# Kernel tuning notes

Measured on AMD Instinct MI355X. Metric: run time of the kernel, lower is better.

## Reference

```python
import jax, jax.numpy as jnp
import numpy as np

B, N, D, H, C = 2, 2048, 1024, 16, 3
Dh = D // H


def setup_inputs() -> dict:
    key = jax.random.key(0)
    ks = jax.random.split(key, 6)
    x = jax.random.normal(ks[0], (B, N, D), jnp.float32)
    coords = jax.random.normal(ks[1], (B, N, C), jnp.float32)
    attn_mask = jax.random.normal(ks[2], (N, N), jnp.float32) * 0.1  # additive float bias (2d kind)
    Wqkv = jax.random.normal(ks[3], (D, 3 * D), jnp.float32) / np.sqrt(D)
    bqkv = jax.random.normal(ks[4], (3 * D,), jnp.float32) * 0.01
    rel_weight = jax.random.normal(ks[5], (H, C), jnp.float32) * 0.02
    return {"x": x, "coords": coords, "attn_mask": attn_mask,
            "Wqkv": Wqkv, "bqkv": bqkv, "rel_weight": rel_weight}


def reference(x, coords, attn_mask, Wqkv, bqkv, rel_weight):
    b, n, d = x.shape
    h, dh = rel_weight.shape[0], d // rel_weight.shape[0]
    scale = 1.0 / np.sqrt(float(dh))

    qkv = x @ Wqkv + bqkv                      # [B,N,3D]
    q, k, v = jnp.split(qkv, 3, axis=-1)

    def to_heads(t):
        return t.reshape(b, n, h, dh).transpose(0, 2, 1, 3)  # [B,H,N,Dh]

    qh, kh, vh = to_heads(q), to_heads(k), to_heads(v)

    # scaled dot-product scores (flex_attention applies scale before score_mod)
    scores = jnp.einsum('bhnd,bhmd->bhnm', qh, kh) * scale   # [B,H,N,N]

    # coordinate-derived per-head relative bias: coord_proj[b,h,qi] - coord_proj[b,h,kj]
    coord_proj = jnp.einsum('bnc,hc->bhn', coords.astype(jnp.float32), rel_weight)
    scores = scores + coord_proj[:, :, :, None] - coord_proj[:, :, None, :]

    # additive float mask bias, '2d' kind: shape (N,N) broadcast over B,H
    scores = scores + attn_mask[None, None, :, :]

    attn = jax.nn.softmax(scores, axis=-1)
    out = jnp.einsum('bhnm,bhmd->bhnd', attn, vh)            # [B,H,N,Dh]
    return out.transpose(0, 2, 1, 3).reshape(b, n, d)        # [B,N,D]
```

## Files before the change

### kernel.cpp

```cpp
#include <hip/hip_runtime.h>

typedef _Float16 half8 __attribute__((ext_vector_type(8)));
typedef _Float16 half4 __attribute__((ext_vector_type(4)));
typedef float floatx4 __attribute__((ext_vector_type(4)));


__device__ __forceinline__ void async16(const void* g, void* l) {
    __builtin_amdgcn_global_load_lds(
        (const __attribute__((address_space(1))) unsigned int*)g,
        (__attribute__((address_space(3))) unsigned int*)l, 16, 0, 0);
}

__global__ void k_convert_x(const float* __restrict__ x, _Float16* __restrict__ xh) {
    int i = blockIdx.x * blockDim.x + threadIdx.x;
    const floatx4* xin = (const floatx4*)x;
    floatx4 a = xin[i * 2];
    floatx4 b = xin[i * 2 + 1];
    half8 h;
    h[0] = (_Float16)a[0]; h[1] = (_Float16)a[1]; h[2] = (_Float16)a[2]; h[3] = (_Float16)a[3];
    h[4] = (_Float16)b[0]; h[5] = (_Float16)b[1]; h[6] = (_Float16)b[2]; h[7] = (_Float16)b[3];
    *(half8*)&xh[i * 8] = h;
}

__global__ void k_transpose_w(const float* __restrict__ W, _Float16* __restrict__ Wt) {
    __shared__ float tile[32][33];
    int n0 = blockIdx.x * 32, k0 = blockIdx.y * 32;
    int tx = threadIdx.x, ty = threadIdx.y;
    #pragma unroll
    for (int r = 0; r < 4; ++r)
        tile[ty + r * 8][tx] = W[(k0 + ty + r * 8) * 3072 + n0 + tx];
    __syncthreads();
    #pragma unroll
    for (int r = 0; r < 4; ++r)
        Wt[(n0 + ty + r * 8) * 1024 + k0 + tx] = (_Float16)tile[tx][ty + r * 8];
}

__global__ void k_negcp(const float* __restrict__ coords, const float* __restrict__ rw,
                        float* __restrict__ negcp) {
    int idx = blockIdx.x * 256 + threadIdx.x;
    int bh = idx >> 11, n = idx & 2047;
    int b = bh >> 4, h = bh & 15;
    const float* c = &coords[(b * 2048 + n) * 3];
    const float* w = &rw[h * 3];
    negcp[idx] = -(c[0] * w[0] + c[1] * w[1] + c[2] * w[2]);
}

__global__ void k_prep_mask(const float* __restrict__ mask, _Float16* __restrict__ maskp) {
    int gid = blockIdx.x * 256 + threadIdx.x;
    int lane = gid & 63, t = (gid >> 6) & 3, w = (gid >> 8) & 3;
    int kt = (gid >> 10) & 31, qt = gid >> 15;
    int quad = lane >> 4, l16 = lane & 15;
    int row = qt * 64 + w * 16 + l16;
    int col = kt * 64 + t * 16 + quad * 4;
    floatx4 m = *(const floatx4*)&mask[row * 2048 + col];
    half4 v;
    #pragma unroll
    for (int i = 0; i < 4; ++i) v[i] = (_Float16)m[i];
    ((half4*)maskp)[gid] = v;
}

__global__ __launch_bounds__(256) void k_gemm(
    const _Float16* __restrict__ Ah, const _Float16* __restrict__ Bt,
    const float* __restrict__ bias,
    _Float16* __restrict__ qh, _Float16* __restrict__ kh, _Float16* __restrict__ vt) {
    __shared__ _Float16 smem[18432];
    _Float16* As = smem;
    _Float16* Bs = smem + 8192;
    int tid = threadIdx.x;
    int w = tid >> 6, lane = tid & 63;
    int quad = lane >> 4, l16 = lane & 15;
    int m0 = blockIdx.y * 128;
    int n0 = blockIdx.x * 128;
    bool QK = n0 < 2048;
    int mq = (w >> 1) * 64, nq = (w & 1) * 64;
    int c0 = n0 + nq;

    int rl = lane >> 3;
    int pb = lane & 7;
    floatx4 acc[4][4] = {};

    for (int kt = 0; kt < 16; ++kt) {
        #pragma unroll
        for (int j = 0; j < 4; ++j) {
            int row = w * 32 + j * 8 + rl;
            async16(&Ah[(size_t)(m0 + row) * 1024 + kt * 64 + ((pb ^ (row & 7)) << 3)],
                    &As[(w * 32 + j * 8) * 64]);
            async16(&Bt[(size_t)(n0 + row) * 1024 + kt * 64 + ((pb ^ (row & 7)) << 3)],
                    &Bs[(w * 32 + j * 8) * 64]);
        }
        __syncthreads();
        #pragma unroll
        for (int kc = 0; kc < 2; ++kc) {
            half8 af[4], bf[4];
            #pragma unroll
            for (int s = 0; s < 4; ++s) {
                int ra = mq + s * 16 + l16;
                af[s] = *(const half8*)&As[ra * 64 + ((((kc << 2) + quad) ^ (ra & 7)) << 3)];
                int rb = nq + s * 16 + l16;
                bf[s] = *(const half8*)&Bs[rb * 64 + ((((kc << 2) + quad) ^ (rb & 7)) << 3)];
            }
            if (QK) {
                #pragma unroll
                for (int ms = 0; ms < 4; ++ms)
                    #pragma unroll
                    for (int ns = 0; ns < 4; ++ns)
                        acc[ms][ns] = __builtin_amdgcn_mfma_f32_16x16x32_f16(bf[ns], af[ms], acc[ms][ns], 0, 0, 0);
            } else {
                #pragma unroll
                for (int ms = 0; ms < 4; ++ms)
                    #pragma unroll
                    for (int ns = 0; ns < 4; ++ns)
                        acc[ms][ns] = __builtin_amdgcn_mfma_f32_16x16x32_f16(af[ms], bf[ns], acc[ms][ns], 0, 0, 0);
            }
        }
        __syncthreads();
    }

    _Float16* Ls = smem + w * 4608;
    int b = (m0 + mq) >> 11, nbase = (m0 + mq) & 2047;
    if (QK) {
        #pragma unroll
        for (int ns = 0; ns < 4; ++ns) {
            floatx4 b4 = *(const floatx4*)&bias[c0 + ns * 16 + quad * 4];
            #pragma unroll
            for (int ms = 0; ms < 4; ++ms) {
                half4 hv;
                #pragma unroll
                for (int i = 0; i < 4; ++i) hv[i] = (_Float16)(acc[ms][ns][i] + b4[i]);
                *(half4*)&Ls[(ms * 16 + l16) * 72 + ns * 16 + quad * 4] = hv;
            }
        }
        int h2 = c0 >> 6;
        _Float16* dst = (h2 < 16 ? qh : kh) + (size_t)(((b << 4) + (h2 & 15)) * 2048) * 64;
        int d0 = pb << 3;
        #pragma unroll
        for (int rep = 0; rep < 8; ++rep) {
            int nl = rep * 8 + rl;
            half8 v = *(const half8*)&Ls[nl * 72 + d0];
            *(half8*)&dst[(size_t)(nbase + nl) * 64 + d0] = v;
        }
    } else {
        #pragma unroll
        for (int ns = 0; ns < 4; ++ns) {
            float bv = bias[c0 + ns * 16 + l16];
            #pragma unroll
            for (int ms = 0; ms < 4; ++ms) {
                half4 hv;
                #pragma unroll
                for (int i = 0; i < 4; ++i) hv[i] = (_Float16)(acc[ms][ns][i] + bv);
                *(half4*)&Ls[(ns * 16 + l16) * 72 + ms * 16 + quad * 4] = hv;
            }
        }
        int h = (c0 - 2048) >> 6;
        _Float16* dst = vt + (size_t)(((b << 4) + h) * 64) * 2048;
        int noff = pb << 3;
        #pragma unroll
        for (int rep = 0; rep < 8; ++rep) {
            int cl = rep * 8 + rl;
            half8 v = *(const half8*)&Ls[cl * 72 + noff];
            *(half8*)&dst[(size_t)cl * 2048 + nbase + noff] = v;
        }
    }
}

__global__ __launch_bounds__(256) void k_attn(
    const _Float16* __restrict__ qh, const _Float16* __restrict__ kh,
    const _Float16* __restrict__ vt, const _Float16* __restrict__ maskp,
    const float* __restrict__ negcp, float* __restrict__ out) {
    __shared__ _Float16 KV[2][8192];
    int tid = threadIdx.x;
    int w = tid >> 6, lane = tid & 63;
    int quad = lane >> 4, l16 = lane & 15;
    int rl = lane >> 3, pb = lane & 7;
    int bid = blockIdx.x;
    int qt = bid & 31, bh = bid >> 5;
    int b = bh >> 4, h = bh & 15;
    int qrow = qt * 64 + w * 16;

    half8 qf[2];
    {
        const _Float16* qp = &qh[((size_t)bh * 2048 + qrow + l16) * 64];
        qf[0] = *(const half8*)&qp[quad * 8];
        qf[1] = *(const half8*)&qp[32 + quad * 8];
    }
    floatx4 o[4] = {};
    float l_part = 0.f;

    const half4* mbase = (const half4*)maskp + (size_t)((qt * 32) * 4 + w) * 4 * 64 + lane;
    const _Float16* khb = kh + (size_t)bh * 2048 * 64;
    const _Float16* vtb = vt + (size_t)bh * 64 * 2048;

    #define STAGE(ktv, buf) {                                                         \
        int kb_ = (ktv) * 64;                                                         \
        _Float16* Kd = &KV[buf][0];                                                   \
        _Float16* Vd = &KV[buf][4096];                                                \
        _Pragma("unroll")                                                             \
        for (int j = 0; j < 2; ++j) {                                                 \
            int row = w * 16 + j * 8 + rl;                                            \
            async16(&khb[(size_t)(kb_ + row) * 64 + ((pb ^ (row & 7)) << 3)],         \
                    &Kd[(w * 16 + j * 8) * 64]);                                      \
            async16(&vtb[(size_t)row * 2048 + kb_ + ((pb ^ (row & 7)) << 3)],         \
                    &Vd[(w * 16 + j * 8) * 64]);                                      \
        }                                                                             \
    }

    STAGE(0, 0);
    for (int kt = 0; kt < 32; ++kt) {
        int cur = kt & 1;
        __syncthreads();
        if (kt < 31) STAGE(kt + 1, cur ^ 1);
        int kb = kt * 64;
        const half4* mp = mbase + (size_t)kt * 1024;
        half4 mload[4];
        floatx4 ncv[4];
        #pragma unroll
        for (int t = 0; t < 4; ++t) mload[t] = mp[t * 64];
        #pragma unroll
        for (int t = 0; t < 4; ++t)
            ncv[t] = *(const floatx4*)&negcp[bh * 2048 + kb + t * 16 + quad * 4];

        const _Float16* Ksc = &KV[cur][0];
        const _Float16* Vsc = &KV[cur][4096];
        floatx4 st[4];
        #pragma unroll
        for (int t = 0; t < 4; ++t) {
            int r = t * 16 + l16;
            half8 k0 = *(const half8*)&Ksc[r * 64 + ((quad ^ (r & 7)) << 3)];
            half8 k1 = *(const half8*)&Ksc[r * 64 + (((quad + 4) ^ (r & 7)) << 3)];
            floatx4 z = {};
            z = __builtin_amdgcn_mfma_f32_16x16x32_f16(k0, qf[0], z, 0, 0, 0);
            z = __builtin_amdgcn_mfma_f32_16x16x32_f16(k1, qf[1], z, 0, 0, 0);
            st[t] = z;
        }
        half4 pt[4];
        #pragma unroll
        for (int t = 0; t < 4; ++t) {
            #pragma unroll
            for (int i = 0; i < 4; ++i) {
                float pv = __expf(fmaf(st[t][i], 0.125f, (float)mload[t][i] + ncv[t][i]));
                l_part += pv;
                pt[t][i] = (_Float16)pv;
            }
        }
        #pragma unroll
        for (int dt = 0; dt < 4; ++dt) {
            int rv = dt * 16 + l16;
            #pragma unroll
            for (int t = 0; t < 4; ++t) {
                half4 vf = *(const half4*)&Vsc[rv * 64 +
                    (((t * 2 + (quad >> 1)) ^ (rv & 7)) << 3) + ((quad & 1) << 2)];
                o[dt] = __builtin_amdgcn_mfma_f32_16x16x16f16(vf, pt[t], o[dt], 0, 0, 0);
            }
        }
    }
    l_part += __shfl_xor(l_part, 16);
    l_part += __shfl_xor(l_part, 32);
    float inv = 1.f / l_part;
    #pragma unroll
    for (int dt = 0; dt < 4; ++dt) {
        floatx4 r;
        #pragma unroll
        for (int i = 0; i < 4; ++i) r[i] = o[dt][i] * inv;
        *(floatx4*)&out[((size_t)(b * 2048 + qrow + l16)) * 1024 + h * 64 + dt * 16 + quad * 4] = r;
    }
    #undef STAGE
}

extern "C" void kernel_launch(void* const* d_in, const int* in_sizes, int n_in,
                              void* d_out, int out_size, void* d_ws, size_t ws_size,
                              hipStream_t stream) {
    const float* x      = (const float*)d_in[0];
    const float* coords = (const float*)d_in[1];
    const float* mask   = (const float*)d_in[2];
    const float* Wqkv   = (const float*)d_in[3];
    const float* bqkv   = (const float*)d_in[4];
    const float* rw     = (const float*)d_in[5];
    float* out = (float*)d_out;

    char* ws = (char*)d_ws;
    _Float16* xh    = (_Float16*)(ws);
    _Float16* maskp = (_Float16*)(ws);
    _Float16* Wt    = (_Float16*)(ws + 8388608);
    _Float16* qh    = (_Float16*)(ws + 14680064);
    _Float16* kh    = (_Float16*)(ws + 23068672);
    _Float16* vt    = (_Float16*)(ws + 31457280);
    float*    ncp   = (float*)(ws + 39845888);

    k_convert_x<<<2048, 256, 0, stream>>>(x, xh);
    k_transpose_w<<<dim3(96, 32), dim3(32, 8), 0, stream>>>(Wqkv, Wt);
    k_negcp<<<256, 256, 0, stream>>>(coords, rw, ncp);
    k_gemm<<<dim3(24, 32), 256, 0, stream>>>(xh, Wt, bqkv, qh, kh, vt);
    k_prep_mask<<<4096, 256, 0, stream>>>(mask, maskp);
    k_attn<<<1024, 256, 0, stream>>>(qh, kh, vt, maskp, ncp, out);
}
```

Baseline: 213.4 us.

## Fold log2e and softmax scale into Q, mask and bias; use exp2 and tidy loops

New measurement: 417.2 us. +95.5%, slower.

```diff
diff --git a/kernel.cpp b/kernel.cpp
--- a/kernel.cpp
+++ b/kernel.cpp
@@ -2,13 +2,23 @@
 
 typedef _Float16 half8 __attribute__((ext_vector_type(8)));
 typedef _Float16 half4 __attribute__((ext_vector_type(4)));
+typedef _Float16 half2v __attribute__((ext_vector_type(2)));
+typedef __fp16 fp16x2 __attribute__((ext_vector_type(2)));
 typedef float floatx4 __attribute__((ext_vector_type(4)));
 
+#define LOG2E 1.44269504088896f
+#define QSCALE 0.18033688011112f
 
 __device__ __forceinline__ void async16(const void* g, void* l) {
     __builtin_amdgcn_global_load_lds(
         (const __attribute__((address_space(1))) unsigned int*)g,
         (__attribute__((address_space(3))) unsigned int*)l, 16, 0, 0);
+}
+__device__ __forceinline__ half4 pack4(float a, float b, float c, float d) {
+    half2v lo = __builtin_bit_cast(half2v, __builtin_amdgcn_cvt_pkrtz(a, b));
+    half2v hi = __builtin_bit_cast(half2v, __builtin_amdgcn_cvt_pkrtz(c, d));
+    half4 r; r[0] = lo[0]; r[1] = lo[1]; r[2] = hi[0]; r[3] = hi[1];
+    return r;
 }
 
 __global__ void k_convert_x(const float* __restrict__ x, _Float16* __restrict__ xh) {
@@ -42,24 +52,30 @@
     int b = bh >> 4, h = bh & 15;
     const float* c = &coords[(b * 2048 + n) * 3];
     const float* w = &rw[h * 3];
-    negcp[idx] = -(c[0] * w[0] + c[1] * w[1] + c[2] * w[2]);
+    negcp[idx] = -LOG2E * (c[0] * w[0] + c[1] * w[1] + c[2] * w[2]);
 }
 
 __global__ void k_prep_mask(const float* __restrict__ mask, _Float16* __restrict__ maskp) {
-    int gid = blockIdx.x * 256 + threadIdx.x;
-    int lane = gid & 63, t = (gid >> 6) & 3, w = (gid >> 8) & 3;
-    int kt = (gid >> 10) & 31, qt = gid >> 15;
-    int quad = lane >> 4, l16 = lane & 15;
-    int row = qt * 64 + w * 16 + l16;
-    int col = kt * 64 + t * 16 + quad * 4;
-    floatx4 m = *(const floatx4*)&mask[row * 2048 + col];
-    half4 v;
-    #pragma unroll
-    for (int i = 0; i < 4; ++i) v[i] = (_Float16)m[i];
-    ((half4*)maskp)[gid] = v;
-}
-
-__global__ __launch_bounds__(256) void k_gemm(
+    __shared__ float tile[64 * 68];
+    int tid = threadIdx.x;
+    int qt = blockIdx.x >> 5, kt = blockIdx.x & 31;
+    int row0 = qt * 64, col0 = kt * 64;
+    int lr = tid >> 2, lc = (tid & 3) * 16;
+    #pragma unroll
+    for (int j = 0; j < 4; ++j)
+        *(floatx4*)&tile[lr * 68 + lc + j * 4] =
+            *(const floatx4*)&mask[(size_t)(row0 + lr) * 2048 + col0 + lc + j * 4];
+    __syncthreads();
+    int w = tid >> 6, lane = tid & 63, quad = lane >> 4, l16 = lane & 15;
+    half4* outp = (half4*)maskp + (size_t)((qt * 32 + kt) * 4 + w) * 256 + lane;
+    #pragma unroll
+    for (int t = 0; t < 4; ++t) {
+        floatx4 m = *(const floatx4*)&tile[(w * 16 + l16) * 68 + t * 16 + quad * 4];
+        outp[t * 64] = pack4(m[0] * LOG2E, m[1] * LOG2E, m[2] * LOG2E, m[3] * LOG2E);
+    }
+}
+
+__global__ __launch_bounds__(256, 4) void k_gemm(
     const _Float16* __restrict__ Ah, const _Float16* __restrict__ Bt,
     const float* __restrict__ bias,
     _Float16* __restrict__ qh, _Float16* __restrict__ kh, _Float16* __restrict__ vt) {
@@ -77,16 +93,24 @@
 
     int rl = lane >> 3;
     int pb = lane & 7;
+    int sw = (pb ^ rl) << 3;
     floatx4 acc[4][4] = {};
 
+    const _Float16* ap[4];
+    const _Float16* bp[4];
+    #pragma unroll
+    for (int j = 0; j < 4; ++j) {
+        int row = w * 32 + j * 8 + rl;
+        ap[j] = Ah + (size_t)(m0 + row) * 1024 + sw;
+        bp[j] = Bt + (size_t)(n0 + row) * 1024 + sw;
+    }
+
     for (int kt = 0; kt < 16; ++kt) {
         #pragma unroll
         for (int j = 0; j < 4; ++j) {
-            int row = w * 32 + j * 8 + rl;
-            async16(&Ah[(size_t)(m0 + row) * 1024 + kt * 64 + ((pb ^ (row & 7)) << 3)],
-                    &As[(w * 32 + j * 8) * 64]);
-            async16(&Bt[(size_t)(n0 + row) * 1024 + kt * 64 + ((pb ^ (row & 7)) << 3)],
-                    &Bs[(w * 32 + j * 8) * 64]);
+            async16(ap[j], &As[(w * 32 + j * 8) * 64]);
+            async16(bp[j], &Bs[(w * 32 + j * 8) * 64]);
+            ap[j] += 64; bp[j] += 64;
         }
         __syncthreads();
         #pragma unroll
@@ -119,15 +143,17 @@
     _Float16* Ls = smem + w * 4608;
     int b = (m0 + mq) >> 11, nbase = (m0 + mq) & 2047;
     if (QK) {
+        float qsc = (c0 < 1024) ? QSCALE : 1.0f;
         #pragma unroll
         for (int ns = 0; ns < 4; ++ns) {
             floatx4 b4 = *(const floatx4*)&bias[c0 + ns * 16 + quad * 4];
             #pragma unroll
             for (int ms = 0; ms < 4; ++ms) {
-                half4 hv;
+                floatx4 v;
                 #pragma unroll
-                for (int i = 0; i < 4; ++i) hv[i] = (_Float16)(acc[ms][ns][i] + b4[i]);
-                *(half4*)&Ls[(ms * 16 + l16) * 72 + ns * 16 + quad * 4] = hv;
+                for (int i = 0; i < 4; ++i) v[i] = (acc[ms][ns][i] + b4[i]) * qsc;
+                *(half4*)&Ls[(ms * 16 + l16) * 72 + ns * 16 + quad * 4] =
+                    pack4(v[0], v[1], v[2], v[3]);
             }
         }
         int h2 = c0 >> 6;
@@ -145,10 +171,9 @@
             float bv = bias[c0 + ns * 16 + l16];
             #pragma unroll
             for (int ms = 0; ms < 4; ++ms) {
-                half4 hv;
-                #pragma unroll
-                for (int i = 0; i < 4; ++i) hv[i] = (_Float16)(acc[ms][ns][i] + bv);
-                *(half4*)&Ls[(ns * 16 + l16) * 72 + ms * 16 + quad * 4] = hv;
+                *(half4*)&Ls[(ns * 16 + l16) * 72 + ms * 16 + quad * 4] =
+                    pack4(acc[ms][ns][0] + bv, acc[ms][ns][1] + bv,
+                          acc[ms][ns][2] + bv, acc[ms][ns][3] + bv);
             }
         }
         int h = (c0 - 2048) >> 6;
@@ -163,7 +188,7 @@
     }
 }
 
-__global__ __launch_bounds__(256) void k_attn(
+__global__ __launch_bounds__(256, 4) void k_attn(
     const _Float16* __restrict__ qh, const _Float16* __restrict__ kh,
     const _Float16* __restrict__ vt, const _Float16* __restrict__ maskp,
     const float* __restrict__ negcp, float* __restrict__ out) {
@@ -186,73 +211,78 @@
     floatx4 o[4] = {};
     float l_part = 0.f;
 
-    const half4* mbase = (const half4*)maskp + (size_t)((qt * 32) * 4 + w) * 4 * 64 + lane;
-    const _Float16* khb = kh + (size_t)bh * 2048 * 64;
-    const _Float16* vtb = vt + (size_t)bh * 64 * 2048;
-
-    #define STAGE(ktv, buf) {                                                         \
-        int kb_ = (ktv) * 64;                                                         \
-        _Float16* Kd = &KV[buf][0];                                                   \
-        _Float16* Vd = &KV[buf][4096];                                                \
-        _Pragma("unroll")                                                             \
-        for (int j = 0; j < 2; ++j) {                                                 \
-            int row = w * 16 + j * 8 + rl;                                            \
-            async16(&khb[(size_t)(kb_ + row) * 64 + ((pb ^ (row & 7)) << 3)],         \
-                    &Kd[(w * 16 + j * 8) * 64]);                                      \
-            async16(&vtb[(size_t)row * 2048 + kb_ + ((pb ^ (row & 7)) << 3)],         \
-                    &Vd[(w * 16 + j * 8) * 64]);                                      \
-        }                                                                             \
-    }
-
-    STAGE(0, 0);
-    for (int kt = 0; kt < 32; ++kt) {
-        int cur = kt & 1;
-        __syncthreads();
-        if (kt < 31) STAGE(kt + 1, cur ^ 1);
-        int kb = kt * 64;
-        const half4* mp = mbase + (size_t)kt * 1024;
-        half4 mload[4];
-        floatx4 ncv[4];
-        #pragma unroll
-        for (int t = 0; t < 4; ++t) mload[t] = mp[t * 64];
-        #pragma unroll
-        for (int t = 0; t < 4; ++t)
-            ncv[t] = *(const floatx4*)&negcp[bh * 2048 + kb + t * 16 + quad * 4];
-
-        const _Float16* Ksc = &KV[cur][0];
-        const _Float16* Vsc = &KV[cur][4096];
-        floatx4 st[4];
-        #pragma unroll
-        for (int t = 0; t < 4; ++t) {
-            int r = t * 16 + l16;
-            half8 k0 = *(const half8*)&Ksc[r * 64 + ((quad ^ (r & 7)) << 3)];
-            half8 k1 = *(const half8*)&Ksc[r * 64 + (((quad + 4) ^ (r & 7)) << 3)];
-            floatx4 z = {};
-            z = __builtin_amdgcn_mfma_f32_16x16x32_f16(k0, qf[0], z, 0, 0, 0);
-            z = __builtin_amdgcn_mfma_f32_16x16x32_f16(k1, qf[1], z, 0, 0, 0);
-            st[t] = z;
-        }
-        half4 pt[4];
-        #pragma unroll
-        for (int t = 0; t < 4; ++t) {
-            #pragma unroll
-            for (int i = 0; i < 4; ++i) {
-                float pv = __expf(fmaf(st[t][i], 0.125f, (float)mload[t][i] + ncv[t][i]));
-                l_part += pv;
-                pt[t][i] = (_Float16)pv;
-            }
-        }
-        #pragma unroll
-        for (int dt = 0; dt < 4; ++dt) {
-            int rv = dt * 16 + l16;
-            #pragma unroll
-            for (int t = 0; t < 4; ++t) {
-                half4 vf = *(const half4*)&Vsc[rv * 64 +
-                    (((t * 2 + (quad >> 1)) ^ (rv & 7)) << 3) + ((quad & 1) << 2)];
-                o[dt] = __builtin_amdgcn_mfma_f32_16x16x16f16(vf, pt[t], o[dt], 0, 0, 0);
-            }
-        }
-    }
+    int sw = (pb ^ rl) << 3;
+    const _Float16* kp0 = kh + (size_t)bh * 131072 + (size_t)(w * 16 + rl) * 64 + sw;
+    const _Float16* kp1 = kp0 + 512;
+    const _Float16* vp0 = vt + (size_t)bh * 131072 + (size_t)(w * 16 + rl) * 2048 + sw;
+    const _Float16* vp1 = vp0 + 16384;
+    const half4* mp = (const half4*)maskp + (size_t)(qt * 128 + w) * 256 + lane;
+    const float* ncpp = negcp + bh * 2048 + quad * 4;
+
+    #define STAGE(buf) {                                             \
+        async16(kp0, &KV[buf][(w * 16) * 64]);                       \
+        async16(kp1, &KV[buf][(w * 16 + 8) * 64]);                   \
+        async16(vp0, &KV[buf][4096 + (w * 16) * 64]);                \
+        async16(vp1, &KV[buf][4096 + (w * 16 + 8) * 64]);            \
+        kp0 += 4096; kp1 += 4096; vp0 += 64; vp1 += 64;              \
+    }
+
+    #define BODY(cur, last) {                                                          \
+        __syncthreads();                                                               \
+        if (!(last)) STAGE((cur) ^ 1);                                                 \
+        half4 mload[4];                                                                \
+        floatx4 ncv[4];                                                                \
+        _Pragma("unroll")                                                              \
+        for (int t = 0; t < 4; ++t) mload[t] = mp[t * 64];                             \
+        _Pragma("unroll")                                                              \
+        for (int t = 0; t < 4; ++t) ncv[t] = *(const floatx4*)&ncpp[t * 16];           \
+        mp += 1024; ncpp += 64;                                                        \
+        const _Float16* Ksc = &KV[cur][0];                                             \
+        const _Float16* Vsc = &KV[cur][4096];                                          \
+        floatx4 st[4];                                                                 \
+        _Pragma("unroll")                                                              \
+        for (int t = 0; t < 4; ++t) {                                                  \
+            int r = t * 16 + l16;                                                      \
+            half8 k0 = *(const half8*)&Ksc[r * 64 + ((quad ^ (r & 7)) << 3)];          \
+            half8 k1 = *(const half8*)&Ksc[r * 64 + (((quad + 4) ^ (r & 7)) << 3)];    \
+            floatx4 z = {};                                                            \
+            z = __builtin_amdgcn_mfma_f32_16x16x32_f16(k0, qf[0], z, 0, 0, 0);         \
+            z = __builtin_amdgcn_mfma_f32_16x16x32_f16(k1, qf[1], z, 0, 0, 0);         \
+            st[t] = z;                                                                 \
+        }                                                                              \
+        half4 pt[4];                                                                   \
+        _Pragma("unroll")                                                              \
+        for (int t = 0; t < 4; ++t) {                                                  \
+            float p0 = exp2f((float)mload[t][0] + ncv[t][0] + st[t][0]);               \
+            float p1 = exp2f((float)mload[t][1] + ncv[t][1] + st[t][1]);               \
+            float p2 = exp2f((float)mload[t][2] + ncv[t][2] + st[t][2]);               \
+            float p3 = exp2f((float)mload[t][3] + ncv[t][3] + st[t][3]);               \
+            l_part += (p0 + p1) + (p2 + p3);                                           \
+            pt[t] = pack4(p0, p1, p2, p3);                                             \
+        }                                                                              \
+        _Pragma("unroll")                                                              \
+        for (int dt = 0; dt < 4; ++dt) {                                               \
+            int rv = dt * 16 + l16;                                                    \
+            _Pragma("unroll")                                                          \
+            for (int t = 0; t < 4; ++t) {                                              \
+                half4 vf = *(const half4*)&Vsc[rv * 64 +                               \
+                    (((t * 2 + (quad >> 1)) ^ (rv & 7)) << 3) + ((quad & 1) << 2)];    \
+                o[dt] = __builtin_amdgcn_mfma_f32_16x16x16f16(vf, pt[t], o[dt], 0, 0, 0); \
+            }                                                                          \
+        }                                                                              \
+    }
+
+    STAGE(0);
+    #pragma unroll 1
+    for (int kt2 = 0; kt2 < 15; ++kt2) {
+        BODY(0, false);
+        BODY(1, false);
+    }
+    BODY(0, false);
+    BODY(1, true);
+    #undef BODY
+    #undef STAGE
+
     l_part += __shfl_xor(l_part, 16);
     l_part += __shfl_xor(l_part, 32);
     float inv = 1.f / l_part;
@@ -263,7 +293,6 @@
         for (int i = 0; i < 4; ++i) r[i] = o[dt][i] * inv;
         *(floatx4*)&out[((size_t)(b * 2048 + qrow + l16)) * 1024 + h * 64 + dt * 16 + quad * 4] = r;
     }
-    #undef STAGE
 }
 
 extern "C" void kernel_launch(void* const* d_in, const int* in_sizes, int n_in,
@@ -290,6 +319,6 @@
     k_transpose_w<<<dim3(96, 32), dim3(32, 8), 0, stream>>>(Wqkv, Wt);
     k_negcp<<<256, 256, 0, stream>>>(coords, rw, ncp);
     k_gemm<<<dim3(24, 32), 256, 0, stream>>>(xh, Wt, bqkv, qh, kh, vt);
-    k_prep_mask<<<4096, 256, 0, stream>>>(mask, maskp);
+    k_prep_mask<<<1024, 256, 0, stream>>>(mask, maskp);
     k_attn<<<1024, 256, 0, stream>>>(qh, kh, vt, maskp, ncp, out);
 }
```
